# Optimization experiments

Hardware: AMD Instinct MI355X
Metric: run time of the kernel (lower is better)

## Reference

```python
import jax, jax.numpy as jnp
import numpy as np

DIM = 1024          # d_model
DI = 2 * DIM        # d_inner (expand=2)
DSTATE = 16         # SSM state size
DCONV = 4           # causal conv width
DTRANK = DIM // 16  # dt_rank = ceil(dim/16) = 64
B_, L = 2, 2048


def setup_inputs() -> dict:
    key = jax.random.key(0)
    ks = jax.random.split(key, 8)
    s = lambda k, shape, sc=0.02: jax.random.normal(k, shape, jnp.float32) * sc
    return {
        "x": jax.random.normal(ks[0], (B_, L, DIM), jnp.float32),
        "ln_w": jnp.ones((DIM,), jnp.float32),
        "ln_b": jnp.zeros((DIM,), jnp.float32),
        "in_proj_w": s(ks[1], (2 * DI, DIM)),
        "conv_w": s(ks[2], (DI, 1, DCONV), 0.1),
        "conv_b": jnp.zeros((DI,), jnp.float32),
        "x_proj_w": s(ks[3], (DTRANK + 2 * DSTATE, DI)),
        "dt_proj_w": s(ks[4], (DI, DTRANK), 0.1),
        # standard Mamba dt bias init: softplus^{-1}(0.01)
        "dt_proj_b": jnp.log(jnp.expm1(jnp.full((DI,), 0.01, jnp.float32))),
        # S4D-real init: A = -[1..d_state]
        "A_log": jnp.log(jnp.broadcast_to(jnp.arange(1, DSTATE + 1, dtype=jnp.float32), (DI, DSTATE))),
        "D": jnp.ones((DI,), jnp.float32),
        "out_proj_w": s(ks[5], (DIM, DI)),
    }


def _layernorm(x, w, b, eps=1e-5):
    mu = x.mean(-1, keepdims=True)
    var = ((x - mu) ** 2).mean(-1, keepdims=True)
    return (x - mu) * jax.lax.rsqrt(var + eps) * w + b


def _silu(x):
    return x * jax.nn.sigmoid(x)


def _mamba(x, in_proj_w, conv_w, conv_b, x_proj_w, dt_proj_w, dt_proj_b, A_log, D, out_proj_w):
    b, l, _ = x.shape
    xz = x @ in_proj_w.T                      # [b,l,2*DI]
    xc, z = jnp.split(xz, 2, axis=-1)
    # depthwise causal conv over time
    xt = jnp.pad(xc.transpose(0, 2, 1), ((0, 0), (0, 0), (DCONV - 1, 0)))
    xt = jax.lax.conv_general_dilated(
        xt, conv_w, (1,), 'VALID',
        dimension_numbers=('NCH', 'OIH', 'NCH'), feature_group_count=DI)
    xc = _silu(xt + conv_b[None, :, None]).transpose(0, 2, 1)  # [b,l,DI]
    # input-dependent dt, B, C
    dbc = xc @ x_proj_w.T
    dt = dbc[..., :DTRANK]
    Bm = dbc[..., DTRANK:DTRANK + DSTATE]     # [b,l,n]
    Cm = dbc[..., DTRANK + DSTATE:]           # [b,l,n]
    delta = jax.nn.softplus(dt @ dt_proj_w.T + dt_proj_b)  # [b,l,DI]
    A = -jnp.exp(A_log)                        # [DI,n]
    dA = jnp.exp(delta[..., None] * A)         # [b,l,DI,n]
    dBu = (delta * xc)[..., None] * Bm[:, :, None, :]  # [b,l,DI,n]

    def step(h, inp):
        dA_t, dBu_t, C_t = inp
        h = dA_t * h + dBu_t                   # [b,DI,n]
        return h, jnp.einsum('bdn,bn->bd', h, C_t)

    h0 = jnp.zeros((b, DI, DSTATE), x.dtype)
    _, ys = jax.lax.scan(step, h0,
                         (dA.transpose(1, 0, 2, 3), dBu.transpose(1, 0, 2, 3), Cm.transpose(1, 0, 2)))
    y = ys.transpose(1, 0, 2) + xc * D         # [b,l,DI]
    y = y * _silu(z)
    return y @ out_proj_w.T


def reference(x, ln_w, ln_b, in_proj_w, conv_w, conv_b, x_proj_w, dt_proj_w, dt_proj_b, A_log, D, out_proj_w):
    # single block: x = x + Mamba(LN(x))
    return x + _mamba(_layernorm(x, ln_w, ln_b), in_proj_w, conv_w, conv_b,
                      x_proj_w, dt_proj_w, dt_proj_b, A_log, D, out_proj_w)
```

## Files before the change

### kernel.cpp

```cpp
#include <hip/hip_runtime.h>
#include <hip/hip_bf16.h>
#include <math.h>

#define DIM 1024
#define DI 2048
#define DSTATE 16
#define DTRANK 64
#define NB 2
#define L_ 2048
#define M_TOT (NB*L_)
#define NCHUNK 64
#define CLEN (L_/NCHUNK)

typedef unsigned short u16;
typedef float f32x4 __attribute__((ext_vector_type(4)));
typedef __bf16 bf16x8 __attribute__((ext_vector_type(8)));

static __device__ __forceinline__ float bf2f(u16 u){
  union{float f;unsigned int i;}x; x.i = ((unsigned int)u)<<16; return x.f;
}
static __device__ __forceinline__ u16 f2bf(float f){
  union{float f;unsigned int u;}v; v.f=f;
  unsigned int x = v.u;
  return (u16)((x + 0x7fffu + ((x>>16)&1u)) >> 16);
}
static __device__ __forceinline__ void gload16(const void* g, void* l){
  __builtin_amdgcn_global_load_lds(
      (const __attribute__((address_space(1))) unsigned int*)g,
      (__attribute__((address_space(3))) unsigned int*)l, 16, 0, 0);
}

#define N4_WIN  1048576
#define N4_WDT  32768
#define N4_WOUT 524288
#define NB_CAST3 ((N4_WIN+N4_WDT+N4_WOUT)/256)
#define NB_XPROJ 256
#define NB_LN    M_TOT
__global__ __launch_bounds__(256) void fused_pre_k(
    const float* __restrict__ in_proj_w, const float* __restrict__ dt_proj_w,
    const float* __restrict__ out_proj_w, const float* __restrict__ x_proj_w,
    const float* __restrict__ x, const float* __restrict__ lw, const float* __restrict__ lb,
    u16* __restrict__ win, u16* __restrict__ wdt, u16* __restrict__ wout,
    u16* __restrict__ wxp, u16* __restrict__ xn){
  const int bid = blockIdx.x, t = threadIdx.x;
  if (bid < NB_CAST3){
    int i = bid*256 + t;
    const float* s; u16* o; int j;
    if (i < N4_WIN){ s = in_proj_w; o = win; j = i; }
    else if (i < N4_WIN+N4_WDT){ s = dt_proj_w; o = wdt; j = i - N4_WIN; }
    else { s = out_proj_w; o = wout; j = i - N4_WIN - N4_WDT; }
    float4 v = reinterpret_cast<const float4*>(s)[j];
    ushort4 ov; ov.x=f2bf(v.x); ov.y=f2bf(v.y); ov.z=f2bf(v.z); ov.w=f2bf(v.w);
    reinterpret_cast<ushort4*>(o)[j] = ov;
    return;
  }
  if (bid < NB_CAST3 + NB_XPROJ){
    int i = (bid - NB_CAST3)*256 + t;
    int row = (i*4) >> 11;
    ushort4 o;
    if (row < 96){
      float4 v = reinterpret_cast<const float4*>(x_proj_w)[i];
      o.x=f2bf(v.x); o.y=f2bf(v.y); o.z=f2bf(v.z); o.w=f2bf(v.w);
    } else { o.x=0;o.y=0;o.z=0;o.w=0; }
    reinterpret_cast<ushort4*>(wxp)[i] = o;
    return;
  }
  const int row = bid - NB_CAST3 - NB_XPROJ;
  const float4 v = reinterpret_cast<const float4*>(x + (size_t)row*DIM)[t];
  float s = v.x+v.y+v.z+v.w;
  float q = v.x*v.x+v.y*v.y+v.z*v.z+v.w*v.w;
  #pragma unroll
  for (int o=1;o<64;o<<=1){ s += __shfl_xor(s,o); q += __shfl_xor(q,o); }
  __shared__ float ss[4], sq[4];
  if ((t&63)==0){ ss[t>>6]=s; sq[t>>6]=q; }
  __syncthreads();
  s = ss[0]+ss[1]+ss[2]+ss[3]; q = sq[0]+sq[1]+sq[2]+sq[3];
  const float mu = s*(1.f/DIM);
  const float rs = rsqrtf(q*(1.f/DIM) - mu*mu + 1e-5f);
  const float4 wv = reinterpret_cast<const float4*>(lw)[t];
  const float4 bv = reinterpret_cast<const float4*>(lb)[t];
  ushort4 o;
  o.x = f2bf((v.x-mu)*rs*wv.x + bv.x);
  o.y = f2bf((v.y-mu)*rs*wv.y + bv.y);
  o.z = f2bf((v.z-mu)*rs*wv.z + bv.z);
  o.w = f2bf((v.w-mu)*rs*wv.w + bv.w);
  reinterpret_cast<ushort4*>(xn + (size_t)row*DIM)[t] = o;
}

template<int MODE, int NSPLIT>
__global__ __launch_bounds__(256,2) void ring_gemm(
    const u16* __restrict__ A, const u16* __restrict__ Bw, int K, int nbn, int nblk,
    float* __restrict__ f0, u16* __restrict__ b0, u16* __restrict__ b1,
    const float* __restrict__ e0){
  constexpr int BM = 128;
  constexpr int TILE_ELEMS = BM*32;
  constexpr int BUF_BYTES = TILE_ELEMS*2*2;
  __shared__ u16 lds0[4*2*TILE_ELEMS];
  const int t = threadIdx.x;
  const int w = t >> 6, lane = t & 63;
  const int lrow = lane & 15;
  const int nwg = gridDim.x;
  int wg = blockIdx.x;
  wg = (wg & 7)*(nwg >> 3) + (wg >> 3);
  const int ks  = (NSPLIT > 1) ? (wg / nblk) : 0;
  const int rem = (NSPLIT > 1) ? (wg % nblk) : wg;
  const int bm = rem / nbn, bn = rem % nbn;
  const int row0 = bm*BM, col0 = bn*BM;
  const int wr = (w>>1)*64, wc = (w&1)*64;
  const int Kpart = K / NSPLIT;
  const int kbase = ks * Kpart;
  const int nt = Kpart >> 5;

  const int srow = t >> 2;
  const int schunk = ((t&3) ^ ((t>>3)&3))*8;
  const u16* gA0 = A + (size_t)(row0 + srow)*K + kbase + schunk;
  const u16* gA1 = gA0 + (size_t)64*K;
  const u16* gB0 = Bw + (size_t)(col0 + srow)*K + kbase + schunk;
  const u16* gB1 = gB0 + (size_t)64*K;
  const int baseA0 = (w*16)*64;
  const int baseA1 = (64 + w*16)*64;
  const int baseB0 = BM*64 + baseA0;
  const int baseB1 = BM*64 + baseA1;

  f32x4 acc[4][4];
  #pragma unroll
  for (int m=0;m<4;m++)
    #pragma unroll
    for (int n=0;n<4;n++) acc[m][n] = (f32x4){0.f,0.f,0.f,0.f};

  const int rchunk = ((lane>>4) ^ ((lane>>1)&3))*8;

  for (int p = 0; p < 3 && p < nt; ++p){
    char* bp = (char*)lds0 + p*BUF_BYTES;
    gload16(gA0, bp + baseA0); gload16(gA1, bp + baseA1);
    gload16(gB0, bp + baseB0); gload16(gB1, bp + baseB1);
    gA0 += 32; gA1 += 32; gB0 += 32; gB1 += 32;
  }

  for (int t2 = 0; t2 < nt; ++t2){
    const int left = nt - 1 - t2;
    if (left >= 2)      asm volatile("s_waitcnt vmcnt(8)" ::: "memory");
    else if (left == 1) asm volatile("s_waitcnt vmcnt(4)" ::: "memory");
    else                asm volatile("s_waitcnt vmcnt(0)" ::: "memory");
    __builtin_amdgcn_s_barrier();
    if (t2 + 3 < nt){
      char* bp = (char*)lds0 + ((t2+3)&3)*BUF_BYTES;
      gload16(gA0, bp + baseA0); gload16(gA1, bp + baseA1);
      gload16(gB0, bp + baseB0); gload16(gB1, bp + baseB1);
      gA0 += 32; gA1 += 32; gB0 += 32; gB1 += 32;
    }
    const u16* Lb = (const u16*)((const char*)lds0 + (t2&3)*BUF_BYTES);
    bf16x8 af[4], bfv[4];
    #pragma unroll
    for (int m=0;m<4;m++)
      af[m] = *reinterpret_cast<const bf16x8*>(&Lb[(wr + m*16 + lrow)*32 + rchunk]);
    #pragma unroll
    for (int n=0;n<4;n++)
      bfv[n] = *reinterpret_cast<const bf16x8*>(&Lb[TILE_ELEMS + (wc + n*16 + lrow)*32 + rchunk]);
    #pragma unroll
    for (int m=0;m<4;m++)
      #pragma unroll
      for (int n=0;n<4;n++)
        acc[m][n] = __builtin_amdgcn_mfma_f32_16x16x32_bf16(af[m], bfv[n], acc[m][n], 0,0,0);
  }

  const int rb = (lane>>4)*4;
  #pragma unroll
  for (int m=0;m<4;m++){
    #pragma unroll
    for (int n=0;n<4;n++){
      #pragma unroll
      for (int i=0;i<4;i++){
        const int row = row0 + wr + m*16 + rb + i;
        const int col = col0 + wc + n*16 + lrow;
        const float v = acc[m][n][i];
        if (MODE==1){
          if (col < DI) b0[(size_t)row*DI + col] = f2bf(v);
          else          b1[(size_t)row*DI + col - DI] = f2bf(v);
        } else if (MODE==3){
          const float xv = v + e0[col];
          const float sp = (xv > 20.f) ? xv : log1pf(__expf(xv));
          b0[(size_t)row*DI + col] = f2bf(sp);
        } else if (MODE==5){
          f0[((size_t)ks*M_TOT + row)*128 + col] = v;
        } else {
          b0[((size_t)ks*M_TOT + row)*1024 + col] = f2bf(v);
        }
      }
    }
  }
}

__global__ __launch_bounds__(256) void reduce_xp_k(const float* __restrict__ P,
    float* __restrict__ dbc, u16* __restrict__ dtb){
  const int tid = blockIdx.x*256 + threadIdx.x;
  const int m = tid >> 5, c4 = tid & 31;
  f32x4 s = (f32x4){0.f,0.f,0.f,0.f};
  #pragma unroll
  for (int k=0;k<8;k++)
    s += *reinterpret_cast<const f32x4*>(&P[((size_t)k*M_TOT + m)*128 + c4*4]);
  *reinterpret_cast<f32x4*>(&dbc[(size_t)m*128 + c4*4]) = s;
  if (c4 < 16){
    ushort4 o; o.x=f2bf(s.x); o.y=f2bf(s.y); o.z=f2bf(s.z); o.w=f2bf(s.w);
    *reinterpret_cast<ushort4*>(&dtb[(size_t)m*DTRANK + c4*4]) = o;
  }
}

__global__ __launch_bounds__(256) void reduce_out_k(const u16* __restrict__ P,
    const float* __restrict__ x, float* __restrict__ out){
  const size_t i = ((size_t)blockIdx.x*256 + threadIdx.x)*4;
  ushort4 a = *reinterpret_cast<const ushort4*>(&P[i]);
  ushort4 b = *reinterpret_cast<const ushort4*>(&P[(size_t)M_TOT*1024 + i]);
  f32x4 xv = *reinterpret_cast<const f32x4*>(&x[i]);
  f32x4 r;
  r.x = bf2f(a.x) + bf2f(b.x) + xv.x;
  r.y = bf2f(a.y) + bf2f(b.y) + xv.y;
  r.z = bf2f(a.z) + bf2f(b.z) + xv.z;
  r.w = bf2f(a.w) + bf2f(b.w) + xv.w;
  *reinterpret_cast<f32x4*>(&out[i]) = r;
}

__global__ __launch_bounds__(256) void conv_silu_k(const u16* __restrict__ xc,
    const float* __restrict__ cw, const float* __restrict__ cb, u16* __restrict__ out){
  const int idx = blockIdx.x*256 + threadIdx.x;
  const int m = idx >> 9;
  const int dq = idx & 511;
  const int d0 = dq*4;
  const int l = m & (L_-1);
  float wgt[4][4];
  #pragma unroll
  for (int j=0;j<4;j++){
    float4 t4 = reinterpret_cast<const float4*>(cw)[d0+j];
    wgt[j][0]=t4.x; wgt[j][1]=t4.y; wgt[j][2]=t4.z; wgt[j][3]=t4.w;
  }
  const float4 bb = reinterpret_cast<const float4*>(cb)[dq];
  float acc[4] = {bb.x, bb.y, bb.z, bb.w};
  #pragma unroll
  for (int k=0;k<4;k++){
    const int ls = l + k - 3;
    if (ls >= 0){
      ushort4 xv = *reinterpret_cast<const ushort4*>(&xc[(size_t)(m+k-3)*DI + d0]);
      float xf[4] = {bf2f(xv.x), bf2f(xv.y), bf2f(xv.z), bf2f(xv.w)};
      #pragma unroll
      for (int j=0;j<4;j++) acc[j] += xf[j]*wgt[j][k];
    }
  }
  ushort4 o;
  u16 ov[4];
  #pragma unroll
  for (int j=0;j<4;j++){
    const float v = acc[j];
    ov[j] = f2bf(v / (1.f + __expf(-v)));
  }
  o.x=ov[0]; o.y=ov[1]; o.z=ov[2]; o.w=ov[3];
  *reinterpret_cast<ushort4*>(&out[(size_t)m*DI + d0]) = o;
}

__global__ __launch_bounds__(256) void scan1_k(const u16* __restrict__ delta,
    const u16* __restrict__ xc, const float* __restrict__ dbc,
    const float* __restrict__ A_log, float* __restrict__ aps, float* __restrict__ hend){
  const int bid = blockIdx.x;
  const int dblk = bid & 7;
  const int bc = bid >> 3;
  const int b = bc >> 6, c = bc & (NCHUNK-1);
  const int t = threadIdx.x;
  const int d = dblk*256 + t;
  __shared__ float Bsh[CLEN*DSTATE];
  const int mbase = b*L_ + c*CLEN;
  Bsh[t]     = dbc[(size_t)(mbase + (t>>4))*128 + 64 + (t&15)];
  Bsh[t+256] = dbc[(size_t)(mbase + 16 + (t>>4))*128 + 64 + (t&15)];
  float un[DSTATE], h[DSTATE];
  #pragma unroll
  for (int n=0;n<DSTATE;n++){
    un[n] = -__expf(A_log[d*DSTATE + n]);
    h[n] = 0.f;
  }
  __syncthreads();
  const u16* dp = delta + (size_t)mbase*DI + d;
  const u16* xp = xc    + (size_t)mbase*DI + d;
  float sdv = 0.f;
  u16 dr = dp[0];
  u16 xr = xp[0];
  for (int j=0;j<CLEN;j++){
    const int jn = (j+1 < CLEN) ? j+1 : j;
    const u16 dr_n = dp[(size_t)jn*DI];
    const u16 xr_n = xp[(size_t)jn*DI];
    const float dv = bf2f(dr);
    const float xf = bf2f(xr);
    sdv += dv;
    const float c0 = dv * xf;
    #pragma unroll
    for (int n=0;n<DSTATE;n++){
      const float dA = __expf(un[n]*dv);
      h[n] = fmaf(dA, h[n], c0 * Bsh[j*DSTATE+n]);
    }
    dr = dr_n; xr = xr_n;
  }
  float* ap_out = aps  + (size_t)bc*(DSTATE*DI) + d;
  float* he_out = hend + (size_t)bc*(DSTATE*DI) + d;
  #pragma unroll
  for (int n=0;n<DSTATE;n++){
    ap_out[(size_t)n*DI] = __expf(un[n]*sdv);
    he_out[(size_t)n*DI] = h[n];
  }
}

__global__ void combine_k(const float* __restrict__ aps, const float* __restrict__ hend,
                          float* __restrict__ hinit){
  const int gid = blockIdx.x*256 + threadIdx.x;
  const int b = gid >> 15;
  const int dn = gid & 32767;
  float h = 0.f;
  #pragma unroll 4
  for (int c=0;c<NCHUNK;c++){
    const size_t idx = (size_t)(b*NCHUNK + c)*(DI*DSTATE) + dn;
    hinit[idx] = h;
    h = hend[idx] + aps[idx]*h;
  }
}

__global__ __launch_bounds__(256) void scan2_k(const u16* __restrict__ delta,
    const u16* __restrict__ xc, const float* __restrict__ dbc,
    const u16* __restrict__ z, const float* __restrict__ A_log, const float* __restrict__ Dvec,
    const float* __restrict__ hinit, u16* __restrict__ y){
  const int bid = blockIdx.x;
  const int dblk = bid & 7;
  const int bc = bid >> 3;
  const int b = bc >> 6, c = bc & (NCHUNK-1);
  const int t = threadIdx.x;
  const int d = dblk*256 + t;
  __shared__ float Bsh[CLEN*DSTATE], Csh[CLEN*DSTATE];
  const int mbase = b*L_ + c*CLEN;
  Bsh[t]     = dbc[(size_t)(mbase + (t>>4))*128 + 64 + (t&15)];
  Bsh[t+256] = dbc[(size_t)(mbase + 16 + (t>>4))*128 + 64 + (t&15)];
  Csh[t]     = dbc[(size_t)(mbase + (t>>4))*128 + 80 + (t&15)];
  Csh[t+256] = dbc[(size_t)(mbase + 16 + (t>>4))*128 + 80 + (t&15)];
  float un[DSTATE], h[DSTATE];
  const float* hi = hinit + (size_t)bc*(DSTATE*DI) + d;
  #pragma unroll
  for (int n=0;n<DSTATE;n++){
    un[n] = -__expf(A_log[d*DSTATE+n]);
    h[n] = hi[(size_t)n*DI];
  }
  const float Dd = Dvec[d];
  __syncthreads();
  const u16* dp = delta + (size_t)mbase*DI + d;
  const u16* xp = xc    + (size_t)mbase*DI + d;
  const u16* zp = z     + (size_t)mbase*DI + d;
  u16* yp = y + (size_t)mbase*DI + d;
  u16 dr = dp[0];
  u16 xr = xp[0], zr = zp[0];
  for (int j=0;j<CLEN;j++){
    const int jn = (j+1 < CLEN) ? j+1 : j;
    const u16 dr_n = dp[(size_t)jn*DI];
    const u16 xr_n = xp[(size_t)jn*DI];
    const u16 zr_n = zp[(size_t)jn*DI];
    const float dv = bf2f(dr);
    const float xf = bf2f(xr), zf = bf2f(zr);
    const float c0 = dv * xf;
    float s = 0.f;
    #pragma unroll
    for (int n=0;n<DSTATE;n++){
      const float dA = __expf(un[n]*dv);
      h[n] = fmaf(dA, h[n], c0 * Bsh[j*DSTATE+n]);
      s = fmaf(h[n], Csh[j*DSTATE+n], s);
    }
    const float yf = fmaf(xf, Dd, s);
    const float yo = yf * (zf / (1.f + __expf(-zf)));
    yp[(size_t)j*DI] = f2bf(yo);
    dr = dr_n; xr = xr_n; zr = zr_n;
  }
}

extern "C" void kernel_launch(void* const* d_in, const int* in_sizes, int n_in,
                              void* d_out, int out_size, void* d_ws, size_t ws_size,
                              hipStream_t stream){
  const float* x         = (const float*)d_in[0];
  const float* ln_w      = (const float*)d_in[1];
  const float* ln_b      = (const float*)d_in[2];
  const float* in_proj_w = (const float*)d_in[3];
  const float* conv_w    = (const float*)d_in[4];
  const float* conv_b    = (const float*)d_in[5];
  const float* x_proj_w  = (const float*)d_in[6];
  const float* dt_proj_w = (const float*)d_in[7];
  const float* dt_proj_b = (const float*)d_in[8];
  const float* A_log     = (const float*)d_in[9];
  const float* Dvec      = (const float*)d_in[10];
  const float* out_proj_w= (const float*)d_in[11];
  float* out = (float*)d_out;

  char* w = (char*)d_ws;
  size_t off = 0;
  auto carve = [&](size_t bytes)->char*{ char* p = w + off; off += (bytes + 255) & ~(size_t)255; return p; };
  u16*   xn    = (u16*)  carve((size_t)M_TOT*DIM*2);
  u16*   win   = (u16*)  carve((size_t)2*DI*DIM*2);
  u16*   xcb   = (u16*)  carve((size_t)M_TOT*DI*2);
  u16*   zb    = (u16*)  carve((size_t)M_TOT*DI*2);
  u16*   xcv   = (u16*)  carve((size_t)M_TOT*DI*2);
  u16*   wxp   = (u16*)  carve((size_t)128*DI*2);
  u16*   dtb   = (u16*)  carve((size_t)M_TOT*DTRANK*2);
  u16*   wdt   = (u16*)  carve((size_t)DI*DTRANK*2);
  u16*   deltab= (u16*)  carve((size_t)M_TOT*DI*2);
  u16*   wout  = (u16*)  carve((size_t)DIM*DI*2);
  u16*   yb    = (u16*)  carve((size_t)M_TOT*DI*2);
  float* Pxp   = (float*)carve((size_t)8*M_TOT*128*4);
  float* dbc   = (float*)carve((size_t)M_TOT*128*4);
  float* aps   = (float*)carve((size_t)NB*NCHUNK*DI*DSTATE*4);
  float* hend  = (float*)carve((size_t)NB*NCHUNK*DI*DSTATE*4);
  float* hinit = (float*)carve((size_t)NB*NCHUNK*DI*DSTATE*4);
  u16* Pout = xcb;

  fused_pre_k<<<NB_CAST3 + NB_XPROJ + NB_LN, 256, 0, stream>>>(
      in_proj_w, dt_proj_w, out_proj_w, x_proj_w, x, ln_w, ln_b,
      win, wdt, wout, wxp, xn);

  ring_gemm<1,1><<<32*32, 256, 0, stream>>>(xn, win, DIM, 32, 1024, nullptr, xcb, zb, nullptr);

  conv_silu_k<<<(M_TOT*512)/256, 256, 0, stream>>>(xcb, conv_w, conv_b, xcv);

  ring_gemm<5,8><<<8*32, 256, 0, stream>>>(xcv, wxp, DI, 1, 32, Pxp, nullptr, nullptr, nullptr);
  reduce_xp_k<<<(M_TOT*32)/256, 256, 0, stream>>>(Pxp, dbc, dtb);

  ring_gemm<3,1><<<32*16, 256, 0, stream>>>(dtb, wdt, DTRANK, 16, 512, nullptr, deltab, nullptr, dt_proj_b);

  scan1_k<<<NB*NCHUNK*8, 256, 0, stream>>>(deltab, xcv, dbc, A_log, aps, hend);
  combine_k<<<(NB*DI*DSTATE)/256, 256, 0, stream>>>(aps, hend, hinit);
  scan2_k<<<NB*NCHUNK*8, 256, 0, stream>>>(deltab, xcv, dbc, zb, A_log, Dvec, hinit, yb);

  ring_gemm<6,2><<<2*32*8, 256, 0, stream>>>(yb, wout, DI, 8, 256, nullptr, Pout, nullptr, nullptr);
  reduce_out_k<<<(M_TOT*1024)/(4*256), 256, 0, stream>>>(Pout, x, out);
}
```

Measured before the change: 248.9 us.

## Add 256x256-tile GEMM kernel for in_proj and out_proj with 4-way split-K

Adds a 512-thread GEMM kernel with 256x256 output tiles, swizzled LDS layout, grouped tile ordering, and MFMA priority boosting. It replaces the 128x128 GEMM for the in_proj and out_proj matmuls, with out_proj now using 4-way split-K. The reduction kernel sums four bf16 partials, and the partial buffer moves to the scan scratch space. Larger tiles raise arithmetic intensity and cut global traffic, but give one block per CU, 256 blocks, and more partial traffic for out_proj.

```diff
diff --git a/kernel.cpp b/kernel.cpp
--- a/kernel.cpp
+++ b/kernel.cpp
@@ -88,9 +88,113 @@
 }
 
 template<int MODE, int NSPLIT>
+__global__ __launch_bounds__(512,1) void ring256(
+    const u16* __restrict__ A, const u16* __restrict__ Bw, int K, int nbn, int nblk,
+    u16* __restrict__ b0, u16* __restrict__ b1){
+  constexpr int TILE = 256*32;
+  constexpr int BUFE = 2*TILE;
+  __shared__ u16 lds[4*BUFE];
+  const int t = threadIdx.x;
+  const int w = t>>6, lane = t&63;
+  const int wr = w>>2, wc = w&3;
+  const int nwg = gridDim.x;
+  int wg = blockIdx.x;
+  wg = (wg&7)*(nwg>>3) + (wg>>3);
+  const int ks  = (NSPLIT>1)? wg/nblk : 0;
+  const int rem = (NSPLIT>1)? wg%nblk : wg;
+  const int SN = nbn>>2;
+  const int s4 = rem>>4, j4 = rem&15;
+  const int bm = (s4/SN)*4 + (j4>>2);
+  const int bn = (s4%SN)*4 + (j4&3);
+  const int row0 = bm*256, col0 = bn*256;
+  const int Kpart = K/NSPLIT, kbase = ks*Kpart, nt = Kpart>>5;
+
+  const int r0 = t>>2;
+  const int cc = (t&3) ^ ((r0>>1)&3);
+  const u16* gA0 = A + (size_t)(row0 + r0)*K + kbase + cc*8;
+  const u16* gA1 = gA0 + (size_t)128*K;
+  const u16* gB0 = Bw + (size_t)(col0 + r0)*K + kbase + cc*8;
+  const u16* gB1 = gB0 + (size_t)128*K;
+  const int baseA0 = (w<<10), baseA1 = (w<<10)+8192;
+  const int baseB0 = 16384+(w<<10), baseB1 = 16384+8192+(w<<10);
+
+  f32x4 acc[8][4];
+  #pragma unroll
+  for (int m=0;m<8;m++)
+    #pragma unroll
+    for (int n=0;n<4;n++) acc[m][n] = (f32x4){0.f,0.f,0.f,0.f};
+
+  int offA[8], offB[4];
+  #pragma unroll
+  for (int m=0;m<8;m++){
+    const int ra = wr*128 + m*16 + (lane&15);
+    offA[m] = ra*32 + (((lane>>4) ^ ((ra>>1)&3))<<3);
+  }
+  #pragma unroll
+  for (int n=0;n<4;n++){
+    const int rb = wc*64 + n*16 + (lane&15);
+    offB[n] = TILE + rb*32 + (((lane>>4) ^ ((rb>>1)&3))<<3);
+  }
+
+  for (int p=0;p<3 && p<nt;++p){
+    char* bp = (char*)lds + (size_t)p*(BUFE*2);
+    gload16(gA0, bp+baseA0); gload16(gA1, bp+baseA1);
+    gload16(gB0, bp+baseB0); gload16(gB1, bp+baseB1);
+    gA0 += 32; gA1 += 32; gB0 += 32; gB1 += 32;
+  }
+
+  for (int t2=0;t2<nt;++t2){
+    const int left = nt-1-t2;
+    if (left>=2)      asm volatile("s_waitcnt vmcnt(8)" ::: "memory");
+    else if (left==1) asm volatile("s_waitcnt vmcnt(4)" ::: "memory");
+    else              asm volatile("s_waitcnt vmcnt(0)" ::: "memory");
+    __builtin_amdgcn_s_barrier();
+    if (t2+3<nt){
+      char* bp = (char*)lds + (size_t)((t2+3)&3)*(BUFE*2);
+      gload16(gA0, bp+baseA0); gload16(gA1, bp+baseA1);
+      gload16(gB0, bp+baseB0); gload16(gB1, bp+baseB1);
+      gA0 += 32; gA1 += 32; gB0 += 32; gB1 += 32;
+    }
+    const u16* Lb = lds + (size_t)(t2&3)*BUFE;
+    bf16x8 af[8], bfv[4];
+    #pragma unroll
+    for (int m=0;m<8;m++) af[m] = *reinterpret_cast<const bf16x8*>(&Lb[offA[m]]);
+    #pragma unroll
+    for (int n=0;n<4;n++) bfv[n] = *reinterpret_cast<const bf16x8*>(&Lb[offB[n]]);
+    __builtin_amdgcn_s_setprio(1);
+    #pragma unroll
+    for (int m=0;m<8;m++)
+      #pragma unroll
+      for (int n=0;n<4;n++)
+        acc[m][n] = __builtin_amdgcn_mfma_f32_16x16x32_bf16(af[m], bfv[n], acc[m][n], 0,0,0);
+    __builtin_amdgcn_s_setprio(0);
+  }
+
+  const int rb4 = (lane>>4)*4, lc = lane&15;
+  #pragma unroll
+  for (int m=0;m<8;m++){
+    #pragma unroll
+    for (int n=0;n<4;n++){
+      #pragma unroll
+      for (int i=0;i<4;i++){
+        const int row = row0 + wr*128 + m*16 + rb4 + i;
+        const int col = col0 + wc*64 + n*16 + lc;
+        const float v = acc[m][n][i];
+        if (MODE==1){
+          if (col < DI) b0[(size_t)row*DI + col] = f2bf(v);
+          else          b1[(size_t)row*DI + col - DI] = f2bf(v);
+        } else {
+          b0[((size_t)ks*M_TOT + row)*1024 + col] = f2bf(v);
+        }
+      }
+    }
+  }
+}
+
+template<int MODE, int NSPLIT>
 __global__ __launch_bounds__(256,2) void ring_gemm(
     const u16* __restrict__ A, const u16* __restrict__ Bw, int K, int nbn, int nblk,
-    float* __restrict__ f0, u16* __restrict__ b0, u16* __restrict__ b1,
+    float* __restrict__ f0, u16* __restrict__ b0,
     const float* __restrict__ e0){
   constexpr int BM = 128;
   constexpr int TILE_ELEMS = BM*32;
@@ -157,11 +261,13 @@
     #pragma unroll
     for (int n=0;n<4;n++)
       bfv[n] = *reinterpret_cast<const bf16x8*>(&Lb[TILE_ELEMS + (wc + n*16 + lrow)*32 + rchunk]);
+    __builtin_amdgcn_s_setprio(1);
     #pragma unroll
     for (int m=0;m<4;m++)
       #pragma unroll
       for (int n=0;n<4;n++)
         acc[m][n] = __builtin_amdgcn_mfma_f32_16x16x32_bf16(af[m], bfv[n], acc[m][n], 0,0,0);
+    __builtin_amdgcn_s_setprio(0);
   }
 
   const int rb = (lane>>4)*4;
@@ -174,17 +280,12 @@
         const int row = row0 + wr + m*16 + rb + i;
         const int col = col0 + wc + n*16 + lrow;
         const float v = acc[m][n][i];
-        if (MODE==1){
-          if (col < DI) b0[(size_t)row*DI + col] = f2bf(v);
-          else          b1[(size_t)row*DI + col - DI] = f2bf(v);
-        } else if (MODE==3){
+        if (MODE==3){
           const float xv = v + e0[col];
           const float sp = (xv > 20.f) ? xv : log1pf(__expf(xv));
           b0[(size_t)row*DI + col] = f2bf(sp);
-        } else if (MODE==5){
+        } else {
           f0[((size_t)ks*M_TOT + row)*128 + col] = v;
-        } else {
-          b0[((size_t)ks*M_TOT + row)*1024 + col] = f2bf(v);
         }
       }
     }
@@ -209,14 +310,12 @@
 __global__ __launch_bounds__(256) void reduce_out_k(const u16* __restrict__ P,
     const float* __restrict__ x, float* __restrict__ out){
   const size_t i = ((size_t)blockIdx.x*256 + threadIdx.x)*4;
-  ushort4 a = *reinterpret_cast<const ushort4*>(&P[i]);
-  ushort4 b = *reinterpret_cast<const ushort4*>(&P[(size_t)M_TOT*1024 + i]);
-  f32x4 xv = *reinterpret_cast<const f32x4*>(&x[i]);
-  f32x4 r;
-  r.x = bf2f(a.x) + bf2f(b.x) + xv.x;
-  r.y = bf2f(a.y) + bf2f(b.y) + xv.y;
-  r.z = bf2f(a.z) + bf2f(b.z) + xv.z;
-  r.w = bf2f(a.w) + bf2f(b.w) + xv.w;
+  f32x4 r = *reinterpret_cast<const f32x4*>(&x[i]);
+  #pragma unroll
+  for (int k=0;k<4;k++){
+    ushort4 a = *reinterpret_cast<const ushort4*>(&P[(size_t)k*M_TOT*1024 + i]);
+    r.x += bf2f(a.x); r.y += bf2f(a.y); r.z += bf2f(a.z); r.w += bf2f(a.w);
+  }
   *reinterpret_cast<f32x4*>(&out[i]) = r;
 }
 
@@ -408,25 +507,25 @@
   float* aps   = (float*)carve((size_t)NB*NCHUNK*DI*DSTATE*4);
   float* hend  = (float*)carve((size_t)NB*NCHUNK*DI*DSTATE*4);
   float* hinit = (float*)carve((size_t)NB*NCHUNK*DI*DSTATE*4);
-  u16* Pout = xcb;
+  u16* Pout = (u16*)aps;
 
   fused_pre_k<<<NB_CAST3 + NB_XPROJ + NB_LN, 256, 0, stream>>>(
       in_proj_w, dt_proj_w, out_proj_w, x_proj_w, x, ln_w, ln_b,
       win, wdt, wout, wxp, xn);
 
-  ring_gemm<1,1><<<32*32, 256, 0, stream>>>(xn, win, DIM, 32, 1024, nullptr, xcb, zb, nullptr);
+  ring256<1,1><<<256, 512, 0, stream>>>(xn, win, DIM, 16, 256, xcb, zb);
 
   conv_silu_k<<<(M_TOT*512)/256, 256, 0, stream>>>(xcb, conv_w, conv_b, xcv);
 
-  ring_gemm<5,8><<<8*32, 256, 0, stream>>>(xcv, wxp, DI, 1, 32, Pxp, nullptr, nullptr, nullptr);
+  ring_gemm<5,8><<<8*32, 256, 0, stream>>>(xcv, wxp, DI, 1, 32, Pxp, nullptr, nullptr);
   reduce_xp_k<<<(M_TOT*32)/256, 256, 0, stream>>>(Pxp, dbc, dtb);
 
-  ring_gemm<3,1><<<32*16, 256, 0, stream>>>(dtb, wdt, DTRANK, 16, 512, nullptr, deltab, nullptr, dt_proj_b);
+  ring_gemm<3,1><<<32*16, 256, 0, stream>>>(dtb, wdt, DTRANK, 16, 512, nullptr, deltab, dt_proj_b);
 
   scan1_k<<<NB*NCHUNK*8, 256, 0, stream>>>(deltab, xcv, dbc, A_log, aps, hend);
   combine_k<<<(NB*DI*DSTATE)/256, 256, 0, stream>>>(aps, hend, hinit);
   scan2_k<<<NB*NCHUNK*8, 256, 0, stream>>>(deltab, xcv, dbc, zb, A_log, Dvec, hinit, yb);
 
-  ring_gemm<6,2><<<2*32*8, 256, 0, stream>>>(yb, wout, DI, 8, 256, nullptr, Pout, nullptr, nullptr);
+  ring256<6,4><<<256, 512, 0, stream>>>(yb, wout, DI, 4, 64, Pout, nullptr);
   reduce_out_k<<<(M_TOT*1024)/(4*256), 256, 0, stream>>>(Pout, x, out);
 }
```

New measurement: 240.4 us. 3.4% less time.
